# Kernel optimization log

Measured on AMD Instinct MI355X. Metric: run time of the kernel, lower is better.

Reference implementation:

```python
import jax, jax.numpy as jnp
import numpy as np

B, N = 1, 320  # embed_dim == seq_len == N is forced by the module's bmm shapes


def setup_inputs() -> dict:
    key = jax.random.key(0)
    k1, k2, k3, k4 = jax.random.split(key, 4)
    s = jax.random.normal(k1, (B, N, N), dtype=jnp.float32)
    futrue = jax.random.normal(k2, (B, N, N, N), dtype=jnp.float32)
    # nn.Linear(embed_dim, embed_dim) params
    lim = 1.0 / np.sqrt(N)
    W = jax.random.uniform(k3, (N, N), minval=-lim, maxval=lim, dtype=jnp.float32)
    b = jax.random.uniform(k4, (N,), minval=-lim, maxval=lim, dtype=jnp.float32)
    return {"s": s, "futrue": futrue, "W": W, "b": b}


def reference(s, futrue, W, b):
    # futrue = self.fc(futrue): Linear on last dim  [B,T,T,E]
    futP = jnp.einsum('bitj,ej->bite', futrue, W) + b
    # fc = s.transpose(1,2) @ futrue : [B,1,E,T] @ [B,T,T,E] -> [B,T,E,E]
    scores = jnp.einsum('bte,bitj->biej', s, futP)
    fc = jax.nn.softmax(scores, axis=-1)          # softmax over last dim
    # vectorized loop: t_i = fc[:, i].sum(1).unsqueeze(-2).bmm(s)
    w = fc.sum(axis=2)                            # [B, T, T] (sum over e)
    out = jnp.einsum('bij,bjk->bik', w, s)        # concat of all t_i -> [B, T, E]
    return out
```

## Files before the change

kernel.cpp:

```cpp
#include <hip/hip_runtime.h>
#include <hip/hip_bf16.h>
#include <math.h>

#define N 320
#define NN (N * N)
#define SST 324
#define ZCNT (NN + N)

typedef float f32x16 __attribute__((ext_vector_type(16)));
typedef short s16x8  __attribute__((ext_vector_type(8)));

#define MFMA32(a, b, c) __builtin_amdgcn_mfma_f32_32x32x16_bf16((a), (b), (c), 0, 0, 0)

union U4V { uint4 q; s16x8 v; };
union UAV { unsigned u[4]; s16x8 v; };

__device__ inline void split2(float x0, float x1, unsigned& hi, unsigned& lo) {
    unsigned u0 = __float_as_uint(x0), u1 = __float_as_uint(x1);
    hi = (u0 >> 16) | (u1 & 0xFFFF0000u);
    float d0 = x0 - __uint_as_float(u0 & 0xFFFF0000u);
    float d1 = x1 - __uint_as_float(u1 & 0xFFFF0000u);
    lo = (__float_as_uint(d0) >> 16) | (__float_as_uint(d1) & 0xFFFF0000u);
}

__global__ __launch_bounds__(256) void zero_w_kernel(float* __restrict__ w) {
    int idx = blockIdx.x * 256 + threadIdx.x;
    if (idx * 4 < ZCNT) ((float4*)w)[idx] = make_float4(0.f, 0.f, 0.f, 0.f);
}

__global__ __launch_bounds__(64) void colsum_kernel(const float* __restrict__ s,
                                                    float* __restrict__ colsum) {
    int e = blockIdx.x * 64 + threadIdx.x;
    int t0 = blockIdx.y * 40;
    float a[8];
#pragma unroll
    for (int u = 0; u < 8; ++u) a[u] = 0.f;
    for (int t = 0; t < 40; t += 8) {
#pragma unroll
        for (int u = 0; u < 8; ++u) a[u] += s[(size_t)(t0 + t + u) * N + e];
    }
    float sum = ((a[0] + a[1]) + (a[2] + a[3])) + ((a[4] + a[5]) + (a[6] + a[7]));
    atomicAdd(&colsum[e], sum);
}

__global__ __launch_bounds__(64) void pack_s_kernel(const float* __restrict__ s,
                                                    uint4* __restrict__ spH,
                                                    uint4* __restrict__ spL) {
    int blk = blockIdx.x;
    int l = threadIdx.x;
    int et = blk / 20, ts = blk % 20;
    int e = et * 32 + (l & 31);
    int t0 = ts * 16 + (l >> 5) * 8;
    unsigned hi[4], lo[4];
#pragma unroll
    for (int d = 0; d < 4; ++d)
        split2(s[(size_t)(t0 + 2 * d) * N + e], s[(size_t)(t0 + 2 * d + 1) * N + e],
               hi[d], lo[d]);
    spH[blk * 64 + l] = make_uint4(hi[0], hi[1], hi[2], hi[3]);
    spL[blk * 64 + l] = make_uint4(lo[0], lo[1], lo[2], lo[3]);
}

__global__ __launch_bounds__(64) void pack_w_kernel(const float* __restrict__ W,
                                                    uint4* __restrict__ wpH,
                                                    uint4* __restrict__ wpL) {
    int blk = blockIdx.x;
    int l = threadIdx.x;
    int jt = blk / 20, ks = blk % 20;
    int j = jt * 32 + (l & 31);
    int k0 = ks * 16 + (l >> 5) * 8;
    const float* wr = W + (size_t)j * N + k0;
    unsigned hi[4], lo[4];
#pragma unroll
    for (int d = 0; d < 4; ++d) split2(wr[2 * d], wr[2 * d + 1], hi[d], lo[d]);
    wpH[blk * 64 + l] = make_uint4(hi[0], hi[1], hi[2], hi[3]);
    wpL[blk * 64 + l] = make_uint4(lo[0], lo[1], lo[2], lo[3]);
}

__global__ __launch_bounds__(640, 5) void fused_kernel(
    const float* __restrict__ fut,
    const uint4* __restrict__ spH, const uint4* __restrict__ spL,
    const uint4* __restrict__ wpH, const uint4* __restrict__ wpL,
    const float* __restrict__ bvec, const float* __restrict__ colsum,
    float* __restrict__ w)
{
    const int bid = blockIdx.x;
    const int i   = (bid / 80) * 8 + (bid & 7);
    const int et  = (bid >> 3) % 10;
    const int tid = threadIdx.x;
    const int wid = tid >> 6;
    const int lane = tid & 63;
    const int l31 = lane & 31;
    const int hf  = lane >> 5;

    __shared__ union {
        unsigned short G[2][40 * 32 * 8];
        float S[32 * SST];
    } sm;
    __shared__ float csh[32];
    __shared__ float Mfin[32];
    __shared__ float Ifin[32];

    if (tid < 32) csh[tid] = colsum[et * 32 + tid];

    f32x16 acc;
#pragma unroll
    for (int r = 0; r < 16; ++r) acc[r] = 0.f;

    const float* fbase = fut + (size_t)i * NN + (size_t)(hf * 8) * N + wid * 32 + l31;
    const uint4* aH = spH + (size_t)(et * 20) * 64 + lane;
    const uint4* aL = spL + (size_t)(et * 20) * 64 + lane;

    for (int ts = 0; ts < 20; ++ts) {
        const float* fp = fbase + (size_t)(ts * 16) * N;
        float f[8];
#pragma unroll
        for (int j = 0; j < 8; ++j) f[j] = fp[j * N];
        U4V ah; ah.q = aH[ts * 64];
        U4V al; al.q = aL[ts * 64];
        UAV bh, bl;
#pragma unroll
        for (int d = 0; d < 4; ++d) split2(f[2 * d], f[2 * d + 1], bh.u[d], bl.u[d]);
        acc = MFMA32(ah.v, bh.v, acc);
        acc = MFMA32(al.v, bh.v, acc);
        acc = MFMA32(ah.v, bl.v, acc);
    }

    {
        const int c  = wid * 4 + (l31 >> 3);
        const int jj = l31 & 7;
        const int sw = c & 7;
        unsigned short* GH = sm.G[0];
        unsigned short* GL = sm.G[1];
#pragma unroll
        for (int r = 0; r < 16; ++r) {
            int e = (r & 3) + ((r >> 2) << 3) + (hf << 2);
            float x = acc[r];
            unsigned u = __float_as_uint(x);
            float d = x - __uint_as_float(u & 0xFFFF0000u);
            int off = (c * 32 + (e ^ sw)) * 8 + jj;
            GH[off] = (unsigned short)(u >> 16);
            GL[off] = (unsigned short)(__float_as_uint(d) >> 16);
        }
    }
    __syncthreads();

    f32x16 acc2;
#pragma unroll
    for (int r = 0; r < 16; ++r) acc2[r] = 0.f;

    const uint4* bH = wpH + (size_t)(wid * 20) * 64 + lane;
    const uint4* bL = wpL + (size_t)(wid * 20) * 64 + lane;
    const unsigned short* GH = sm.G[0];
    const unsigned short* GL = sm.G[1];

#pragma unroll 4
    for (int ks = 0; ks < 20; ++ks) {
        int c0 = ks * 2 + hf;
        int aoff = (c0 * 32 + (l31 ^ (c0 & 7))) * 8;
        s16x8 gah = *(const s16x8*)&GH[aoff];
        s16x8 gal = *(const s16x8*)&GL[aoff];
        U4V wh; wh.q = bH[ks * 64];
        U4V wl; wl.q = bL[ks * 64];
        acc2 = MFMA32(gah, wh.v, acc2);
        acc2 = MFMA32(gal, wh.v, acc2);
        acc2 = MFMA32(gah, wl.v, acc2);
    }

    const int jcol = wid * 32 + l31;
    float bj = bvec[jcol];
    float v[16];
#pragma unroll
    for (int r = 0; r < 16; ++r) {
        int e = (r & 3) + ((r >> 2) << 3) + (hf << 2);
        v[r] = acc2[r] + csh[e] * bj;
    }

    __syncthreads();

#pragma unroll
    for (int r = 0; r < 16; ++r) {
        int e = (r & 3) + ((r >> 2) << 3) + (hf << 2);
        sm.S[e * SST + jcol] = v[r];
    }
    __syncthreads();

    const int hw = tid >> 5;
    const int li = tid & 31;
    if (hw < 16) {
#pragma unroll
        for (int rr = 0; rr < 2; ++rr) {
            int row = 2 * hw + rr;
            float x[10];
            float m = -3.4e38f;
#pragma unroll
            for (int q = 0; q < 10; ++q) {
                x[q] = sm.S[row * SST + li + 32 * q];
                m = fmaxf(m, x[q]);
            }
#pragma unroll
            for (int off = 16; off; off >>= 1) m = fmaxf(m, __shfl_xor(m, off, 64));
            float ssum = 0.f;
#pragma unroll
            for (int q = 0; q < 10; ++q) ssum += __expf(x[q] - m);
#pragma unroll
            for (int off = 16; off; off >>= 1) ssum += __shfl_xor(ssum, off, 64);
            if (li == 0) { Mfin[row] = m; Ifin[row] = 1.0f / ssum; }
        }
    }
    __syncthreads();

    float wcol = 0.f;
#pragma unroll
    for (int r = 0; r < 16; ++r) {
        int e = (r & 3) + ((r >> 2) << 3) + (hf << 2);
        wcol += __expf(v[r] - Mfin[e]) * Ifin[e];
    }
    wcol += __shfl_xor(wcol, 32, 64);
    if (hf == 0) atomicAdd(&w[(size_t)i * N + jcol], wcol);
}

__global__ __launch_bounds__(320) void out_gemm_kernel(
    const float* __restrict__ w, const float* __restrict__ s,
    float* __restrict__ out)
{
    const int i = blockIdx.x;
    const int k = threadIdx.x;
    const float* wr = w + (size_t)i * N;
    float a0 = 0.f, a1 = 0.f, a2 = 0.f, a3 = 0.f;
    for (int j = 0; j < N; j += 4) {
        a0 += wr[j + 0] * s[(size_t)(j + 0) * N + k];
        a1 += wr[j + 1] * s[(size_t)(j + 1) * N + k];
        a2 += wr[j + 2] * s[(size_t)(j + 2) * N + k];
        a3 += wr[j + 3] * s[(size_t)(j + 3) * N + k];
    }
    out[(size_t)i * N + k] = (a0 + a1) + (a2 + a3);
}

extern "C" void kernel_launch(void* const* d_in, const int* in_sizes, int n_in,
                              void* d_out, int out_size, void* d_ws, size_t ws_size,
                              hipStream_t stream)
{
    const float* s    = (const float*)d_in[0];
    const float* fut  = (const float*)d_in[1];
    const float* W    = (const float*)d_in[2];
    const float* bvec = (const float*)d_in[3];
    float* out = (float*)d_out;

    char* base = (char*)d_ws;
    float* wbuf   = (float*)base;
    float* colsum = (float*)(base + 409600);
    uint4* spH = (uint4*)(base + 410880);
    uint4* spL = (uint4*)(base + 615680);
    uint4* wpH = (uint4*)(base + 820480);
    uint4* wpL = (uint4*)(base + 1025280);

    zero_w_kernel<<<dim3((ZCNT / 4 + 255) / 256), dim3(256), 0, stream>>>(wbuf);
    colsum_kernel<<<dim3(5, 8), dim3(64), 0, stream>>>(s, colsum);
    pack_s_kernel<<<dim3(200), dim3(64), 0, stream>>>(s, spH, spL);
    pack_w_kernel<<<dim3(200), dim3(64), 0, stream>>>(W, wpH, wpL);

    fused_kernel<<<dim3(3200), dim3(640), 0, stream>>>(
        fut, spH, spL, wpH, wpL, bvec, colsum, wbuf);

    out_gemm_kernel<<<dim3(N), dim3(320), 0, stream>>>(wbuf, s, out);
}
```

Baseline: 386.7 us.

## Merge prep kernels, software-pipeline fused loads, split output GEMM with atomics

Four small prep launches (zeroing, column sums, s and W packing) become a single prep kernel. Column sums are now written as partial sums and reduced inside the fused kernel instead of through atomics. The fused kernel's two MFMA loops are software-pipelined so the next tile's global and LDS loads are issued before the current tile's MFMAs, and the W-packed load is hoisted ahead of the shared-memory staging. The output GEMM is split four ways along j with atomicAdd into a pre-zeroed output, which raises parallelism but adds atomics and makes the summation order nondeterministic.

```diff
diff --git a/kernel.cpp b/kernel.cpp
--- a/kernel.cpp
+++ b/kernel.cpp
@@ -5,7 +5,6 @@
 #define N 320
 #define NN (N * N)
 #define SST 324
-#define ZCNT (NN + N)
 
 typedef float f32x16 __attribute__((ext_vector_type(16)));
 typedef short s16x8  __attribute__((ext_vector_type(8)));
@@ -23,64 +22,64 @@
     lo = (__float_as_uint(d0) >> 16) | (__float_as_uint(d1) & 0xFFFF0000u);
 }
 
-__global__ __launch_bounds__(256) void zero_w_kernel(float* __restrict__ w) {
-    int idx = blockIdx.x * 256 + threadIdx.x;
-    if (idx * 4 < ZCNT) ((float4*)w)[idx] = make_float4(0.f, 0.f, 0.f, 0.f);
-}
-
-__global__ __launch_bounds__(64) void colsum_kernel(const float* __restrict__ s,
-                                                    float* __restrict__ colsum) {
-    int e = blockIdx.x * 64 + threadIdx.x;
-    int t0 = blockIdx.y * 40;
-    float a[8];
-#pragma unroll
-    for (int u = 0; u < 8; ++u) a[u] = 0.f;
-    for (int t = 0; t < 40; t += 8) {
-#pragma unroll
-        for (int u = 0; u < 8; ++u) a[u] += s[(size_t)(t0 + t + u) * N + e];
-    }
-    float sum = ((a[0] + a[1]) + (a[2] + a[3])) + ((a[4] + a[5]) + (a[6] + a[7]));
-    atomicAdd(&colsum[e], sum);
-}
-
-__global__ __launch_bounds__(64) void pack_s_kernel(const float* __restrict__ s,
-                                                    uint4* __restrict__ spH,
-                                                    uint4* __restrict__ spL) {
-    int blk = blockIdx.x;
-    int l = threadIdx.x;
-    int et = blk / 20, ts = blk % 20;
-    int e = et * 32 + (l & 31);
-    int t0 = ts * 16 + (l >> 5) * 8;
-    unsigned hi[4], lo[4];
-#pragma unroll
-    for (int d = 0; d < 4; ++d)
-        split2(s[(size_t)(t0 + 2 * d) * N + e], s[(size_t)(t0 + 2 * d + 1) * N + e],
-               hi[d], lo[d]);
-    spH[blk * 64 + l] = make_uint4(hi[0], hi[1], hi[2], hi[3]);
-    spL[blk * 64 + l] = make_uint4(lo[0], lo[1], lo[2], lo[3]);
-}
-
-__global__ __launch_bounds__(64) void pack_w_kernel(const float* __restrict__ W,
-                                                    uint4* __restrict__ wpH,
-                                                    uint4* __restrict__ wpL) {
-    int blk = blockIdx.x;
-    int l = threadIdx.x;
-    int jt = blk / 20, ks = blk % 20;
-    int j = jt * 32 + (l & 31);
-    int k0 = ks * 16 + (l >> 5) * 8;
-    const float* wr = W + (size_t)j * N + k0;
-    unsigned hi[4], lo[4];
-#pragma unroll
-    for (int d = 0; d < 4; ++d) split2(wr[2 * d], wr[2 * d + 1], hi[d], lo[d]);
-    wpH[blk * 64 + l] = make_uint4(hi[0], hi[1], hi[2], hi[3]);
-    wpL[blk * 64 + l] = make_uint4(lo[0], lo[1], lo[2], lo[3]);
+__global__ __launch_bounds__(256) void prep_kernel(
+    const float* __restrict__ s, const float* __restrict__ W,
+    float* __restrict__ wbuf, float* __restrict__ out, float* __restrict__ cpart,
+    uint4* __restrict__ spH, uint4* __restrict__ spL,
+    uint4* __restrict__ wpH, uint4* __restrict__ wpL)
+{
+    const int bid = blockIdx.x;
+    const int tid = threadIdx.x;
+    if (bid < 100) {
+        ((float4*)wbuf)[bid * 256 + tid] = make_float4(0.f, 0.f, 0.f, 0.f);
+    } else if (bid < 200) {
+        ((float4*)out)[(bid - 100) * 256 + tid] = make_float4(0.f, 0.f, 0.f, 0.f);
+    } else if (bid < 210) {
+        int idx = (bid - 200) * 256 + tid;
+        int e = idx % N;
+        int chunk = idx / N;
+        const float* sp = s + (size_t)chunk * 40 * N + e;
+        float a[8];
+#pragma unroll
+        for (int u = 0; u < 8; ++u) a[u] = 0.f;
+        for (int t = 0; t < 40; t += 8) {
+#pragma unroll
+            for (int u = 0; u < 8; ++u) a[u] += sp[(size_t)(t + u) * N];
+        }
+        cpart[idx] = ((a[0] + a[1]) + (a[2] + a[3])) + ((a[4] + a[5]) + (a[6] + a[7]));
+    } else if (bid < 260) {
+        int sub = (bid - 210) * 4 + (tid >> 6);
+        int l = tid & 63;
+        int et = sub / 20, ts = sub % 20;
+        int e = et * 32 + (l & 31);
+        int t0 = ts * 16 + (l >> 5) * 8;
+        unsigned hi[4], lo[4];
+#pragma unroll
+        for (int d = 0; d < 4; ++d)
+            split2(s[(size_t)(t0 + 2 * d) * N + e], s[(size_t)(t0 + 2 * d + 1) * N + e],
+                   hi[d], lo[d]);
+        spH[sub * 64 + l] = make_uint4(hi[0], hi[1], hi[2], hi[3]);
+        spL[sub * 64 + l] = make_uint4(lo[0], lo[1], lo[2], lo[3]);
+    } else {
+        int sub = (bid - 260) * 4 + (tid >> 6);
+        int l = tid & 63;
+        int jt = sub / 20, ks = sub % 20;
+        int j = jt * 32 + (l & 31);
+        int k0 = ks * 16 + (l >> 5) * 8;
+        const float* wr = W + (size_t)j * N + k0;
+        unsigned hi[4], lo[4];
+#pragma unroll
+        for (int d = 0; d < 4; ++d) split2(wr[2 * d], wr[2 * d + 1], hi[d], lo[d]);
+        wpH[sub * 64 + l] = make_uint4(hi[0], hi[1], hi[2], hi[3]);
+        wpL[sub * 64 + l] = make_uint4(lo[0], lo[1], lo[2], lo[3]);
+    }
 }
 
 __global__ __launch_bounds__(640, 5) void fused_kernel(
     const float* __restrict__ fut,
     const uint4* __restrict__ spH, const uint4* __restrict__ spL,
     const uint4* __restrict__ wpH, const uint4* __restrict__ wpL,
-    const float* __restrict__ bvec, const float* __restrict__ colsum,
+    const float* __restrict__ bvec, const float* __restrict__ cpart,
     float* __restrict__ w)
 {
     const int bid = blockIdx.x;
@@ -100,30 +99,63 @@
     __shared__ float Mfin[32];
     __shared__ float Ifin[32];
 
-    if (tid < 32) csh[tid] = colsum[et * 32 + tid];
+    if (tid < 32) {
+        float c = 0.f;
+#pragma unroll
+        for (int q = 0; q < 8; ++q) c += cpart[q * N + et * 32 + tid];
+        csh[tid] = c;
+    }
 
     f32x16 acc;
 #pragma unroll
     for (int r = 0; r < 16; ++r) acc[r] = 0.f;
 
     const float* fbase = fut + (size_t)i * NN + (size_t)(hf * 8) * N + wid * 32 + l31;
-    const uint4* aH = spH + (size_t)(et * 20) * 64 + lane;
-    const uint4* aL = spL + (size_t)(et * 20) * 64 + lane;
-
-    for (int ts = 0; ts < 20; ++ts) {
-        const float* fp = fbase + (size_t)(ts * 16) * N;
-        float f[8];
-#pragma unroll
-        for (int j = 0; j < 8; ++j) f[j] = fp[j * N];
-        U4V ah; ah.q = aH[ts * 64];
-        U4V al; al.q = aL[ts * 64];
+    const uint4* aHp = spH + (size_t)(et * 20) * 64 + lane;
+    const uint4* aLp = spL + (size_t)(et * 20) * 64 + lane;
+
+    float f[8];
+    U4V ah, al;
+    {
+#pragma unroll
+        for (int j = 0; j < 8; ++j) f[j] = fbase[(size_t)j * N];
+        ah.q = aHp[0];
+        al.q = aLp[0];
+    }
+    for (int ts = 0; ts < 19; ++ts) {
+        float fn[8];
+        const float* fp = fbase + (size_t)((ts + 1) * 16) * N;
+#pragma unroll
+        for (int j = 0; j < 8; ++j) fn[j] = fp[(size_t)j * N];
+        U4V ahn, aln;
+        ahn.q = aHp[(ts + 1) * 64];
+        aln.q = aLp[(ts + 1) * 64];
+
         UAV bh, bl;
 #pragma unroll
         for (int d = 0; d < 4; ++d) split2(f[2 * d], f[2 * d + 1], bh.u[d], bl.u[d]);
         acc = MFMA32(ah.v, bh.v, acc);
         acc = MFMA32(al.v, bh.v, acc);
         acc = MFMA32(ah.v, bl.v, acc);
-    }
+
+#pragma unroll
+        for (int j = 0; j < 8; ++j) f[j] = fn[j];
+        ah = ahn; al = aln;
+    }
+    {
+        UAV bh, bl;
+#pragma unroll
+        for (int d = 0; d < 4; ++d) split2(f[2 * d], f[2 * d + 1], bh.u[d], bl.u[d]);
+        acc = MFMA32(ah.v, bh.v, acc);
+        acc = MFMA32(al.v, bh.v, acc);
+        acc = MFMA32(ah.v, bl.v, acc);
+    }
+
+    const uint4* bHp = wpH + (size_t)(wid * 20) * 64 + lane;
+    const uint4* bLp = wpL + (size_t)(wid * 20) * 64 + lane;
+    U4V wh, wl;
+    wh.q = bHp[0];
+    wl.q = bLp[0];
 
     {
         const int c  = wid * 4 + (l31 >> 3);
@@ -148,19 +180,33 @@
 #pragma unroll
     for (int r = 0; r < 16; ++r) acc2[r] = 0.f;
 
-    const uint4* bH = wpH + (size_t)(wid * 20) * 64 + lane;
-    const uint4* bL = wpL + (size_t)(wid * 20) * 64 + lane;
     const unsigned short* GH = sm.G[0];
     const unsigned short* GL = sm.G[1];
 
-#pragma unroll 4
-    for (int ks = 0; ks < 20; ++ks) {
-        int c0 = ks * 2 + hf;
+    s16x8 gah, gal;
+    {
+        int c0 = hf;
         int aoff = (c0 * 32 + (l31 ^ (c0 & 7))) * 8;
-        s16x8 gah = *(const s16x8*)&GH[aoff];
-        s16x8 gal = *(const s16x8*)&GL[aoff];
-        U4V wh; wh.q = bH[ks * 64];
-        U4V wl; wl.q = bL[ks * 64];
+        gah = *(const s16x8*)&GH[aoff];
+        gal = *(const s16x8*)&GL[aoff];
+    }
+    for (int ks = 0; ks < 19; ++ks) {
+        U4V whn, wln;
+        whn.q = bHp[(ks + 1) * 64];
+        wln.q = bLp[(ks + 1) * 64];
+        int c1 = (ks + 1) * 2 + hf;
+        int aoff1 = (c1 * 32 + (l31 ^ (c1 & 7))) * 8;
+        s16x8 gahn = *(const s16x8*)&GH[aoff1];
+        s16x8 galn = *(const s16x8*)&GL[aoff1];
+
+        acc2 = MFMA32(gah, wh.v, acc2);
+        acc2 = MFMA32(gal, wh.v, acc2);
+        acc2 = MFMA32(gah, wl.v, acc2);
+
+        gah = gahn; gal = galn;
+        wh = whn; wl = wln;
+    }
+    {
         acc2 = MFMA32(gah, wh.v, acc2);
         acc2 = MFMA32(gal, wh.v, acc2);
         acc2 = MFMA32(gah, wl.v, acc2);
@@ -224,16 +270,18 @@
     float* __restrict__ out)
 {
     const int i = blockIdx.x;
+    const int jc = blockIdx.y;
     const int k = threadIdx.x;
-    const float* wr = w + (size_t)i * N;
+    const float* wr = w + (size_t)i * N + jc * 80;
+    const float* sp = s + (size_t)(jc * 80) * N + k;
     float a0 = 0.f, a1 = 0.f, a2 = 0.f, a3 = 0.f;
-    for (int j = 0; j < N; j += 4) {
-        a0 += wr[j + 0] * s[(size_t)(j + 0) * N + k];
-        a1 += wr[j + 1] * s[(size_t)(j + 1) * N + k];
-        a2 += wr[j + 2] * s[(size_t)(j + 2) * N + k];
-        a3 += wr[j + 3] * s[(size_t)(j + 3) * N + k];
-    }
-    out[(size_t)i * N + k] = (a0 + a1) + (a2 + a3);
+    for (int j = 0; j < 80; j += 4) {
+        a0 += wr[j + 0] * sp[(size_t)(j + 0) * N];
+        a1 += wr[j + 1] * sp[(size_t)(j + 1) * N];
+        a2 += wr[j + 2] * sp[(size_t)(j + 2) * N];
+        a3 += wr[j + 3] * sp[(size_t)(j + 3) * N];
+    }
+    atomicAdd(&out[(size_t)i * N + k], (a0 + a1) + (a2 + a3));
 }
 
 extern "C" void kernel_launch(void* const* d_in, const int* in_sizes, int n_in,
@@ -247,20 +295,18 @@
     float* out = (float*)d_out;
 
     char* base = (char*)d_ws;
-    float* wbuf   = (float*)base;
-    float* colsum = (float*)(base + 409600);
-    uint4* spH = (uint4*)(base + 410880);
-    uint4* spL = (uint4*)(base + 615680);
-    uint4* wpH = (uint4*)(base + 820480);
-    uint4* wpL = (uint4*)(base + 1025280);
-
-    zero_w_kernel<<<dim3((ZCNT / 4 + 255) / 256), dim3(256), 0, stream>>>(wbuf);
-    colsum_kernel<<<dim3(5, 8), dim3(64), 0, stream>>>(s, colsum);
-    pack_s_kernel<<<dim3(200), dim3(64), 0, stream>>>(s, spH, spL);
-    pack_w_kernel<<<dim3(200), dim3(64), 0, stream>>>(W, wpH, wpL);
+    float* wbuf  = (float*)base;
+    float* cpart = (float*)(base + 409600);
+    uint4* spH = (uint4*)(base + 419840);
+    uint4* spL = (uint4*)(base + 624640);
+    uint4* wpH = (uint4*)(base + 829440);
+    uint4* wpL = (uint4*)(base + 1034240);
+
+    prep_kernel<<<dim3(310), dim3(256), 0, stream>>>(
+        s, W, wbuf, out, cpart, spH, spL, wpH, wpL);
 
     fused_kernel<<<dim3(3200), dim3(640), 0, stream>>>(
-        fut, spH, spL, wpH, wpL, bvec, colsum, wbuf);
-
-    out_gemm_kernel<<<dim3(N), dim3(320), 0, stream>>>(wbuf, s, out);
-}
+        fut, spH, spL, wpH, wpL, bvec, cpart, wbuf);
+
+    out_gemm_kernel<<<dim3(320, 4), dim3(320), 0, stream>>>(wbuf, s, out);
+}
```

New measurement: 368.8 us. -4.6%, faster.
